# Optimization experiments

Measured on AMD Instinct MI355X. Metric: run time of the kernel, lower is better.

The kernel has to match this reference:

```python
import jax, jax.numpy as jnp
import numpy as np
from jax import lax

SEQ, B, IN, H, NLAYERS, OUT_LEN, OUT_SIZE = 80, 32768, 2, 10, 2, 20, 2


def _lstm_layer(x, h0, c0, Wih, Whh, bih, bhh):
    """PyTorch-convention LSTM layer. x: [T,B,F], h0/c0: [B,H]. Returns [T,B,H]."""
    b = bih + bhh  # [4H]

    def step(carry, xt):
        h, c = carry
        gates = xt @ Wih.T + h @ Whh.T + b  # [B,4H], gate order i,f,g,o
        i, f, g, o = jnp.split(gates, 4, axis=-1)
        i = jax.nn.sigmoid(i)
        f = jax.nn.sigmoid(f)
        g = jnp.tanh(g)
        o = jax.nn.sigmoid(o)
        c = f * c + i * g
        h = o * jnp.tanh(c)
        return (h, c), h

    (_, _), ys = lax.scan(step, (h0, c0), x)
    return ys


def setup_inputs() -> dict:
    key = jax.random.key(0)
    ks = jax.random.split(key, 16)
    s = 1.0 / np.sqrt(H)  # torch default init scale
    u = lambda k, shp: jax.random.uniform(k, shp, jnp.float32, -s, s)
    inp = {
        "x": jax.random.normal(ks[0], (SEQ, B, IN), jnp.float32),
        "h0": jnp.zeros((NLAYERS, B, H), jnp.float32),
        "c0": jnp.zeros((NLAYERS, B, H), jnp.float32),
        # layer 0 LSTM params
        "Wih0": u(ks[1], (4 * H, IN)),
        "Whh0": u(ks[2], (4 * H, H)),
        "bih0": u(ks[3], (4 * H,)),
        "bhh0": u(ks[4], (4 * H,)),
        # layer 1 LSTM params
        "Wih1": u(ks[5], (4 * H, H)),
        "Whh1": u(ks[6], (4 * H, H)),
        "bih1": u(ks[7], (4 * H,)),
        "bhh1": u(ks[8], (4 * H,)),
        # MLP head: Linear(800 -> 10), Sigmoid, Linear(10 -> 40)
        "W1": jax.random.uniform(ks[9], (H, SEQ * H), jnp.float32, -1 / np.sqrt(SEQ * H), 1 / np.sqrt(SEQ * H)),
        "b1": jax.random.uniform(ks[10], (H,), jnp.float32, -1 / np.sqrt(SEQ * H), 1 / np.sqrt(SEQ * H)),
        "W2": u(ks[11], (OUT_LEN * OUT_SIZE, H)),
        "b2": u(ks[12], (OUT_LEN * OUT_SIZE,)),
    }
    return inp


def reference(x, h0, c0, Wih0, Whh0, bih0, bhh0, Wih1, Whh1, bih1, bhh1, W1, b1, W2, b2):
    y0 = _lstm_layer(x, h0[0], c0[0], Wih0, Whh0, bih0, bhh0)   # [T,B,H]
    y1 = _lstm_layer(y0, h0[1], c0[1], Wih1, Whh1, bih1, bhh1)  # [T,B,H]
    out = jnp.tanh(y1)
    out = out.reshape(B, -1)  # faithful to torch .view(batch, -1) on [T,B,H]
    out = jax.nn.sigmoid(out @ W1.T + b1)
    out = out @ W2.T + b2  # [B, OUT_LEN*OUT_SIZE]
    return out.reshape(OUT_LEN, B, OUT_SIZE)
```

## Files before the change

### kernel.cpp

```cpp
#include <hip/hip_runtime.h>
#include <hip/hip_fp16.h>

#define SEQ   80
#define BATCH 32768
#define HID   10

typedef unsigned int uint;
typedef unsigned short ushort;
typedef _Float16 f16;
typedef __attribute__((ext_vector_type(8))) _Float16 f16x8;
typedef __attribute__((ext_vector_type(2))) _Float16 f16x2;
typedef __attribute__((ext_vector_type(2))) __fp16 fp16x2;
typedef __attribute__((ext_vector_type(4))) float f32x4;

#define SIG_SCALE  (-1.44269504f)
#define TANH_SCALE (-2.88539008f)

__device__ __forceinline__ float fast_rcp(float x)  { return __builtin_amdgcn_rcpf(x); }
__device__ __forceinline__ float fast_exp2(float x) { return __builtin_amdgcn_exp2f(x); }
__device__ __forceinline__ float sigp(float a)  { return fast_rcp(1.0f + fast_exp2(a)); }
__device__ __forceinline__ float tanhp(float a) { return 2.0f * fast_rcp(1.0f + fast_exp2(a)) - 1.0f; }
__device__ __forceinline__ float tanh_f(float x){ return tanhp(TANH_SCALE * x); }

union U4V { uint4 u; f16x8 v; };
union UH2 { uint u; f16x2 h; fp16x2 p; };
union HU  { f16 h; ushort s; };

__device__ __forceinline__ float lstm_unit(const f32x4 d, float& c) {
    const float Ei = fast_exp2(d[0]);
    const float Ef = fast_exp2(d[1]);
    const float Eg = fast_exp2(d[2]);
    const float Eo = fast_exp2(d[3]);
    const float Pi = 1.0f + Ei, Pf = 1.0f + Ef, Pg = 1.0f + Eg;
    const float PiPg = Pi * Pg;
    const float R = fast_rcp(PiPg * Pf);
    c = c * (PiPg * R) + ((1.0f - Eg) * Pf) * R;
    const float Ec = fast_exp2(TANH_SCALE * c);
    const float R2 = fast_rcp((1.0f + Eo) * (1.0f + Ec));
    return (1.0f - Ec) * R2;
}

__global__ __launch_bounds__(128, 4)
void lstm2_spec(const float* __restrict__ x, const float* __restrict__ h0in,
                const float* __restrict__ c0in,
                const float* __restrict__ Wih0, const float* __restrict__ Whh0,
                const float* __restrict__ bih0, const float* __restrict__ bhh0,
                const float* __restrict__ Wih1, const float* __restrict__ Whh1,
                const float* __restrict__ bih1, const float* __restrict__ bhh1,
                ushort* __restrict__ y ) {
    __shared__ __align__(16) ushort buf[3][16][40];
    const int tid  = threadIdx.x;
    const int l    = tid & 63;
    const int role = tid >> 6;
    const int bl   = l & 15;
    const int grp  = l >> 4;
    const long b   = (long)blockIdx.x * 16 + bl;

    f16x8 A[3];
    f32x4 bs[3];
#pragma unroll
    for (int T = 0; T < 3; ++T) {
        const int R  = 16 * T + bl;
        const int u  = R >> 2, gi = R & 3;
        const bool vr = (R < 40);
        const int tr = gi * 10 + u;
        const float sc = (gi == 2) ? TANH_SCALE : SIG_SCALE;
#pragma unroll
        for (int j = 0; j < 8; ++j) {
            const int k = grp * 8 + j;
            float w = 0.f;
            if (vr) {
                if (role == 0) {
                    if (k < 10)      w = Whh0[tr * 10 + k];
                    else if (k < 12) w = Wih0[tr * 2 + (k - 10)];
                } else {
                    if (k < 10)      w = Wih1[tr * 10 + k];
                    else if (k < 20) w = Whh1[tr * 10 + (k - 10)];
                }
            }
            A[T][j] = (f16)(w * sc);
        }
#pragma unroll
        for (int q = 0; q < 4; ++q) {
            const int Rc = 16 * T + grp * 4 + q;
            const int uc = Rc >> 2, gc = Rc & 3;
            const float scc = (gc == 2) ? TANH_SCALE : SIG_SCALE;
            const int trc = gc * 10 + uc;
            float bb = 0.f;
            if (Rc < 40)
                bb = (role == 0) ? (bih0[trc] + bhh0[trc]) : (bih1[trc] + bhh1[trc]);
            bs[T][q] = bb * scc;
        }
    }

    const size_t cbase = (role == 0) ? 0 : (size_t)BATCH * 10;
    float cS[3];
#pragma unroll
    for (int T = 0; T < 3; ++T) {
        const int u = 4 * T + grp;
        cS[T] = (u < 10) ? c0in[cbase + b * 10 + u] : 0.f;
    }

    {
        uint* p = (uint*)buf;
        for (int idx = tid; idx < 960; idx += 128) p[idx] = 0u;
    }
    __syncthreads();
    if (role == 0) {
        ushort* row = &buf[2][bl][0];
#pragma unroll
        for (int T = 0; T < 3; ++T) {
            const int u = 4 * T + grp;
            if (u < 10) { HU h; h.h = (f16)h0in[b * 10 + u]; row[u] = h.s; }
        }
    } else {
        ushort* row = &buf[0][bl][0];
#pragma unroll
        for (int T = 0; T < 3; ++T) {
            const int u = 4 * T + grp;
            if (u < 10) { HU h; h.h = (f16)h0in[(size_t)BATCH * 10 + b * 10 + u]; row[10 + u] = h.s; }
        }
    }

    const float* xq = x + b * 2 + (size_t)BATCH * 2;
    float2 xv = make_float2(0.f, 0.f);
    if (role == 0) xv = *reinterpret_cast<const float2*>(x + b * 2);
    ushort* yq = y + b * HID;

    const uint mx  = (grp < 2)  ? 0xFFFFFFFFu : 0u;
    const uint my0 = (grp == 0) ? 0xFFFFFFFFu : 0u;
    const uint sx  = (grp == 1) ? 0xFFFFFFFFu : 0u;

    auto body = [&](int i, ushort (*W)[40], const ushort (*Rb)[40]) {
        __syncthreads();
        if (role == 0) {
            if (i < SEQ) {
                const float2 xnext = *reinterpret_cast<const float2*>(xq);
                U4V r; r.u = *reinterpret_cast<const uint4*>(&Rb[bl][0] + grp * 8);
                UH2 xp; xp.p = __builtin_amdgcn_cvt_pkrtz(xv.x, xv.y);
                U4V bv;
                bv.u.x = r.u.x & mx;
                bv.u.y = (r.u.y & my0) | (xp.u & sx);
                bv.u.z = r.u.z & my0;
                bv.u.w = r.u.w & my0;

                const f32x4 d0 = __builtin_amdgcn_mfma_f32_16x16x32_f16(A[0], bv.v, bs[0], 0, 0, 0);
                const f32x4 d1 = __builtin_amdgcn_mfma_f32_16x16x32_f16(A[1], bv.v, bs[1], 0, 0, 0);
                const f32x4 d2 = __builtin_amdgcn_mfma_f32_16x16x32_f16(A[2], bv.v, bs[2], 0, 0, 0);

                HU hA; hA.h = (f16)lstm_unit(d0, cS[0]);
                HU hB; hB.h = (f16)lstm_unit(d1, cS[1]);
                HU hC; hC.h = (f16)lstm_unit(d2, cS[2]);

                ushort* wrow = &W[bl][0];
                wrow[grp]     = hA.s;
                wrow[4 + grp] = hB.s;
                if (grp < 2) wrow[8 + grp] = hC.s;

                xv = xnext;
                if (i + 2 < SEQ) xq += (size_t)BATCH * 2;
            }
        } else {
            if (i >= 1) {
                U4V r; r.u = *reinterpret_cast<const uint4*>(&Rb[bl][0] + grp * 8);

                const f32x4 d0 = __builtin_amdgcn_mfma_f32_16x16x32_f16(A[0], r.v, bs[0], 0, 0, 0);
                const f32x4 d1 = __builtin_amdgcn_mfma_f32_16x16x32_f16(A[1], r.v, bs[1], 0, 0, 0);
                const f32x4 d2 = __builtin_amdgcn_mfma_f32_16x16x32_f16(A[2], r.v, bs[2], 0, 0, 0);

                HU hA; hA.h = (f16)lstm_unit(d0, cS[0]);
                HU hB; hB.h = (f16)lstm_unit(d1, cS[1]);
                HU hC; hC.h = (f16)lstm_unit(d2, cS[2]);

                ushort* wrow = &W[bl][0];
                wrow[10 + grp] = hA.s;
                wrow[14 + grp] = hB.s;
                if (grp < 2) wrow[18 + grp] = hC.s;

                yq[grp]     = hA.s;
                yq[4 + grp] = hB.s;
                if (grp < 2) yq[8 + grp] = hC.s;
                yq += (size_t)BATCH * HID;
            }
        }
    };

    for (int i0 = 0; i0 < 81; i0 += 3) {
        body(i0 + 0, buf[0], buf[2]);
        body(i0 + 1, buf[1], buf[0]);
        body(i0 + 2, buf[2], buf[1]);
    }
}

__global__ __launch_bounds__(256, 2)
void head_mfma(const ushort* __restrict__ yflat,
               const float* __restrict__ W1, const float* __restrict__ b1,
               const float* __restrict__ W2, const float* __restrict__ b2,
               float* __restrict__ out) {
    __shared__ float sbuf[4][16][12];
    const int tid = threadIdx.x;
    const int l   = tid & 63;
    const int wv  = tid >> 6;
    const int bl  = l & 15;
    const int grp = l >> 4;
    const long row = ((long)blockIdx.x * 4 + wv) * 16 + bl;

    const ushort* yrow = yflat + row * 800;
    const float* arow = W1 + (size_t)(bl < 10 ? bl : 9) * 800;

    f32x4 acc = {0.f, 0.f, 0.f, 0.f};
#pragma unroll 5
    for (int c = 0; c < 25; ++c) {
        U4V bv; bv.u = *reinterpret_cast<const uint4*>(yrow + c * 32 + grp * 8);
        f16x8 tv;
#pragma unroll
        for (int e = 0; e < 8; ++e)
            tv[e] = (f16)tanh_f((float)bv.v[e]);
        const float4 w0 = *reinterpret_cast<const float4*>(arow + c * 32 + grp * 8);
        const float4 w1 = *reinterpret_cast<const float4*>(arow + c * 32 + grp * 8 + 4);
        f16x8 af;
        af[0] = (f16)w0.x; af[1] = (f16)w0.y; af[2] = (f16)w0.z; af[3] = (f16)w0.w;
        af[4] = (f16)w1.x; af[5] = (f16)w1.y; af[6] = (f16)w1.z; af[7] = (f16)w1.w;
        acc = __builtin_amdgcn_mfma_f32_16x16x32_f16(af, tv, acc, 0, 0, 0);
    }

#pragma unroll
    for (int q = 0; q < 4; ++q) {
        const int o = grp * 4 + q;
        if (o < 10)
            sbuf[wv][bl][o] = sigp(SIG_SCALE * (acc[q] + b1[o]));
    }

    float s[10];
#pragma unroll
    for (int o = 0; o < 10; ++o) s[o] = sbuf[wv][bl][o];

    float* op = out + row * 40 + grp * 10;
#pragma unroll
    for (int jj = 0; jj < 10; ++jj) {
        const int j = grp * 10 + jj;
        float r = b2[j];
#pragma unroll
        for (int o = 0; o < 10; ++o) r += s[o] * W2[j * 10 + o];
        op[jj] = r;
    }
}

extern "C" void kernel_launch(void* const* d_in, const int* in_sizes, int n_in,
                              void* d_out, int out_size, void* d_ws, size_t ws_size,
                              hipStream_t stream) {
    const float* x    = (const float*)d_in[0];
    const float* h0   = (const float*)d_in[1];
    const float* c0   = (const float*)d_in[2];
    const float* Wih0 = (const float*)d_in[3];
    const float* Whh0 = (const float*)d_in[4];
    const float* bih0 = (const float*)d_in[5];
    const float* bhh0 = (const float*)d_in[6];
    const float* Wih1 = (const float*)d_in[7];
    const float* Whh1 = (const float*)d_in[8];
    const float* bih1 = (const float*)d_in[9];
    const float* bhh1 = (const float*)d_in[10];
    const float* W1   = (const float*)d_in[11];
    const float* b1   = (const float*)d_in[12];
    const float* W2   = (const float*)d_in[13];
    const float* b2   = (const float*)d_in[14];
    float* out = (float*)d_out;
    ushort* yws = (ushort*)d_ws;

    lstm2_spec<<<2048, 128, 0, stream>>>(x, h0, c0, Wih0, Whh0, bih0, bhh0,
                                         Wih1, Whh1, bih1, bhh1, yws);
    head_mfma<<<512, 256, 0, stream>>>(yws, W1, b1, W2, b2, out);
}
```

Before: 102.3 us.

## Split LSTM gate tiles across six waves and split head K-loop across wave pairs

The LSTM kernel now uses 384 threads per block, so each of three waves per layer handles one 16-row gate tile (one MFMA and one cell update per step) instead of one wave doing all three tiles serially. This shortens the per-step dependent chain and exposes more wave-level parallelism, at the cost of more waves contending at each per-step barrier and more threads per block. The head kernel splits the 25-chunk reduction between two waves per row group, combining partial sums through shared memory with an added barrier, and launches twice the blocks. Lanes with grp 2-3 in the head now write duplicate outputs, which is redundant but harmless.

```diff
diff --git a/kernel.cpp b/kernel.cpp
--- a/kernel.cpp
+++ b/kernel.cpp
@@ -40,30 +40,33 @@
     return (1.0f - Ec) * R2;
 }
 
-__global__ __launch_bounds__(128, 4)
-void lstm2_spec(const float* __restrict__ x, const float* __restrict__ h0in,
-                const float* __restrict__ c0in,
-                const float* __restrict__ Wih0, const float* __restrict__ Whh0,
-                const float* __restrict__ bih0, const float* __restrict__ bhh0,
-                const float* __restrict__ Wih1, const float* __restrict__ Whh1,
-                const float* __restrict__ bih1, const float* __restrict__ bhh1,
-                ushort* __restrict__ y ) {
+__global__ __launch_bounds__(384)
+void lstm2_spec6(const float* __restrict__ x, const float* __restrict__ h0in,
+                 const float* __restrict__ c0in,
+                 const float* __restrict__ Wih0, const float* __restrict__ Whh0,
+                 const float* __restrict__ bih0, const float* __restrict__ bhh0,
+                 const float* __restrict__ Wih1, const float* __restrict__ Whh1,
+                 const float* __restrict__ bih1, const float* __restrict__ bhh1,
+                 ushort* __restrict__ y ) {
     __shared__ __align__(16) ushort buf[3][16][40];
     const int tid  = threadIdx.x;
     const int l    = tid & 63;
-    const int role = tid >> 6;
+    const int wid  = tid >> 6;
+    const int role = wid >= 3;
+    const int T    = wid - role * 3;
     const int bl   = l & 15;
     const int grp  = l >> 4;
+    const int u    = 4 * T + grp;
+    const bool uok = (u < 10);
     const long b   = (long)blockIdx.x * 16 + bl;
 
-    f16x8 A[3];
-    f32x4 bs[3];
-#pragma unroll
-    for (int T = 0; T < 3; ++T) {
+    f16x8 A;
+    f32x4 bs;
+    {
         const int R  = 16 * T + bl;
-        const int u  = R >> 2, gi = R & 3;
+        const int ru = R >> 2, gi = R & 3;
         const bool vr = (R < 40);
-        const int tr = gi * 10 + u;
+        const int tr = gi * 10 + ru;
         const float sc = (gi == 2) ? TANH_SCALE : SIG_SCALE;
 #pragma unroll
         for (int j = 0; j < 8; ++j) {
@@ -78,7 +81,7 @@
                     else if (k < 20) w = Whh1[tr * 10 + (k - 10)];
                 }
             }
-            A[T][j] = (f16)(w * sc);
+            A[j] = (f16)(w * sc);
         }
 #pragma unroll
         for (int q = 0; q < 4; ++q) {
@@ -89,43 +92,28 @@
             float bb = 0.f;
             if (Rc < 40)
                 bb = (role == 0) ? (bih0[trc] + bhh0[trc]) : (bih1[trc] + bhh1[trc]);
-            bs[T][q] = bb * scc;
+            bs[q] = bb * scc;
         }
     }
 
     const size_t cbase = (role == 0) ? 0 : (size_t)BATCH * 10;
-    float cS[3];
-#pragma unroll
-    for (int T = 0; T < 3; ++T) {
-        const int u = 4 * T + grp;
-        cS[T] = (u < 10) ? c0in[cbase + b * 10 + u] : 0.f;
-    }
+    float cS = uok ? c0in[cbase + b * 10 + u] : 0.f;
 
     {
         uint* p = (uint*)buf;
-        for (int idx = tid; idx < 960; idx += 128) p[idx] = 0u;
+        for (int idx = tid; idx < 960; idx += 384) p[idx] = 0u;
     }
     __syncthreads();
     if (role == 0) {
-        ushort* row = &buf[2][bl][0];
-#pragma unroll
-        for (int T = 0; T < 3; ++T) {
-            const int u = 4 * T + grp;
-            if (u < 10) { HU h; h.h = (f16)h0in[b * 10 + u]; row[u] = h.s; }
-        }
+        if (uok) { HU h; h.h = (f16)h0in[b * 10 + u]; buf[2][bl][u] = h.s; }
     } else {
-        ushort* row = &buf[0][bl][0];
-#pragma unroll
-        for (int T = 0; T < 3; ++T) {
-            const int u = 4 * T + grp;
-            if (u < 10) { HU h; h.h = (f16)h0in[(size_t)BATCH * 10 + b * 10 + u]; row[10 + u] = h.s; }
-        }
+        if (uok) { HU h; h.h = (f16)h0in[(size_t)BATCH * 10 + b * 10 + u]; buf[0][bl][10 + u] = h.s; }
     }
 
     const float* xq = x + b * 2 + (size_t)BATCH * 2;
     float2 xv = make_float2(0.f, 0.f);
     if (role == 0) xv = *reinterpret_cast<const float2*>(x + b * 2);
-    ushort* yq = y + b * HID;
+    ushort* yq = y + b * HID + u;
 
     const uint mx  = (grp < 2)  ? 0xFFFFFFFFu : 0u;
     const uint my0 = (grp == 0) ? 0xFFFFFFFFu : 0u;
@@ -144,18 +132,9 @@
                 bv.u.z = r.u.z & my0;
                 bv.u.w = r.u.w & my0;
 
-                const f32x4 d0 = __builtin_amdgcn_mfma_f32_16x16x32_f16(A[0], bv.v, bs[0], 0, 0, 0);
-                const f32x4 d1 = __builtin_amdgcn_mfma_f32_16x16x32_f16(A[1], bv.v, bs[1], 0, 0, 0);
-                const f32x4 d2 = __builtin_amdgcn_mfma_f32_16x16x32_f16(A[2], bv.v, bs[2], 0, 0, 0);
-
-                HU hA; hA.h = (f16)lstm_unit(d0, cS[0]);
-                HU hB; hB.h = (f16)lstm_unit(d1, cS[1]);
-                HU hC; hC.h = (f16)lstm_unit(d2, cS[2]);
-
-                ushort* wrow = &W[bl][0];
-                wrow[grp]     = hA.s;
-                wrow[4 + grp] = hB.s;
-                if (grp < 2) wrow[8 + grp] = hC.s;
+                const f32x4 d = __builtin_amdgcn_mfma_f32_16x16x32_f16(A, bv.v, bs, 0, 0, 0);
+                HU h; h.h = (f16)lstm_unit(d, cS);
+                if (uok) W[bl][u] = h.s;
 
                 xv = xnext;
                 if (i + 2 < SEQ) xq += (size_t)BATCH * 2;
@@ -164,22 +143,12 @@
             if (i >= 1) {
                 U4V r; r.u = *reinterpret_cast<const uint4*>(&Rb[bl][0] + grp * 8);
 
-                const f32x4 d0 = __builtin_amdgcn_mfma_f32_16x16x32_f16(A[0], r.v, bs[0], 0, 0, 0);
-                const f32x4 d1 = __builtin_amdgcn_mfma_f32_16x16x32_f16(A[1], r.v, bs[1], 0, 0, 0);
-                const f32x4 d2 = __builtin_amdgcn_mfma_f32_16x16x32_f16(A[2], r.v, bs[2], 0, 0, 0);
-
-                HU hA; hA.h = (f16)lstm_unit(d0, cS[0]);
-                HU hB; hB.h = (f16)lstm_unit(d1, cS[1]);
-                HU hC; hC.h = (f16)lstm_unit(d2, cS[2]);
-
-                ushort* wrow = &W[bl][0];
-                wrow[10 + grp] = hA.s;
-                wrow[14 + grp] = hB.s;
-                if (grp < 2) wrow[18 + grp] = hC.s;
-
-                yq[grp]     = hA.s;
-                yq[4 + grp] = hB.s;
-                if (grp < 2) yq[8 + grp] = hC.s;
+                const f32x4 d = __builtin_amdgcn_mfma_f32_16x16x32_f16(A, r.v, bs, 0, 0, 0);
+                HU h; h.h = (f16)lstm_unit(d, cS);
+                if (uok) {
+                    W[bl][10 + u] = h.s;
+                    *yq = h.s;
+                }
                 yq += (size_t)BATCH * HID;
             }
         }
@@ -197,20 +166,24 @@
                const float* __restrict__ W1, const float* __restrict__ b1,
                const float* __restrict__ W2, const float* __restrict__ b2,
                float* __restrict__ out) {
-    __shared__ float sbuf[4][16][12];
-    const int tid = threadIdx.x;
-    const int l   = tid & 63;
-    const int wv  = tid >> 6;
-    const int bl  = l & 15;
-    const int grp = l >> 4;
-    const long row = ((long)blockIdx.x * 4 + wv) * 16 + bl;
+    __shared__ float sbuf[2][2][16][12];
+    const int tid  = threadIdx.x;
+    const int l    = tid & 63;
+    const int wv   = tid >> 6;
+    const int rg   = wv >> 1;
+    const int half = wv & 1;
+    const int bl   = l & 15;
+    const int grp  = l >> 4;
+    const long row = ((long)blockIdx.x * 2 + rg) * 16 + bl;
 
     const ushort* yrow = yflat + row * 800;
     const float* arow = W1 + (size_t)(bl < 10 ? bl : 9) * 800;
 
+    const int c0 = half ? 13 : 0;
+    const int c1 = half ? 25 : 13;
+
     f32x4 acc = {0.f, 0.f, 0.f, 0.f};
-#pragma unroll 5
-    for (int c = 0; c < 25; ++c) {
+    for (int c = c0; c < c1; ++c) {
         U4V bv; bv.u = *reinterpret_cast<const uint4*>(yrow + c * 32 + grp * 8);
         f16x8 tv;
 #pragma unroll
@@ -228,17 +201,20 @@
     for (int q = 0; q < 4; ++q) {
         const int o = grp * 4 + q;
         if (o < 10)
-            sbuf[wv][bl][o] = sigp(SIG_SCALE * (acc[q] + b1[o]));
-    }
+            sbuf[rg][half][bl][o] = acc[q];
+    }
+    __syncthreads();
 
     float s[10];
 #pragma unroll
-    for (int o = 0; o < 10; ++o) s[o] = sbuf[wv][bl][o];
-
-    float* op = out + row * 40 + grp * 10;
+    for (int o = 0; o < 10; ++o)
+        s[o] = sigp(SIG_SCALE * (sbuf[rg][0][bl][o] + sbuf[rg][1][bl][o] + b1[o]));
+
+    const int jbase = half * 20 + (grp & 1) * 10;
+    float* op = out + row * 40 + jbase;
 #pragma unroll
     for (int jj = 0; jj < 10; ++jj) {
-        const int j = grp * 10 + jj;
+        const int j = jbase + jj;
         float r = b2[j];
 #pragma unroll
         for (int o = 0; o < 10; ++o) r += s[o] * W2[j * 10 + o];
@@ -267,7 +243,7 @@
     float* out = (float*)d_out;
     ushort* yws = (ushort*)d_ws;
 
-    lstm2_spec<<<2048, 128, 0, stream>>>(x, h0, c0, Wih0, Whh0, bih0, bhh0,
-                                         Wih1, Whh1, bih1, bhh1, yws);
-    head_mfma<<<512, 256, 0, stream>>>(yws, W1, b1, W2, b2, out);
-}
+    lstm2_spec6<<<2048, 384, 0, stream>>>(x, h0, c0, Wih0, Whh0, bih0, bhh0,
+                                          Wih1, Whh1, bih1, bhh1, yws);
+    head_mfma<<<1024, 256, 0, stream>>>(yws, W1, b1, W2, b2, out);
+}
```

Result: slower. 110.1 us (+7.6%).
